# Performance work log

Hardware: AMD Instinct MI355X
Metric: run time of the kernel (lower is better)

## Reference

```python
import jax, jax.numpy as jnp
import numpy as np

TOPK = 100  # hardcoded in Block: kNNAttention(..., topk=100)
EPS = 1e-5  # torch LayerNorm default


def layer_norm(x, w, b):
    m = jnp.mean(x, axis=-1, keepdims=True)
    v = jnp.mean(jnp.square(x - m), axis=-1, keepdims=True)
    return (x - m) * jax.lax.rsqrt(v + EPS) * w + b


def setup_inputs() -> dict:
    key = jax.random.key(0)
    ks = jax.random.split(key, 8)
    B, N, C, H = 32, 512, 768, 12
    hid = 4 * C
    s_in = 1.0 / np.sqrt(C)
    s_hid = 1.0 / np.sqrt(hid)
    return {
        "x": jax.random.normal(ks[0], (B, N, C), jnp.float32),
        "islast": 0,
        "ln1_w": jnp.ones((C,), jnp.float32),
        "ln1_b": jnp.zeros((C,), jnp.float32),
        "qkv_w": jax.random.normal(ks[1], (3 * C, C), jnp.float32) * s_in,  # qkv_bias=False
        "proj_w": jax.random.normal(ks[2], (C, C), jnp.float32) * s_in,
        "proj_b": jnp.zeros((C,), jnp.float32),
        "ln2_w": jnp.ones((C,), jnp.float32),
        "ln2_b": jnp.zeros((C,), jnp.float32),
        "fc1_w": jax.random.normal(ks[3], (hid, C), jnp.float32) * s_in,
        "fc1_b": jnp.zeros((hid,), jnp.float32),
        "fc2_w": jax.random.normal(ks[4], (C, hid), jnp.float32) * s_hid,
        "fc2_b": jnp.zeros((C,), jnp.float32),
    }


def reference(x, islast, ln1_w, ln1_b, qkv_w, proj_w, proj_b, ln2_w, ln2_b, fc1_w, fc1_b, fc2_w, fc2_b):
    B, N, C = x.shape
    H = 12
    D = C // H
    scale = D ** -0.5

    # --- kNN attention on norm1(x) ---
    xn = layer_norm(x, ln1_w, ln1_b)
    qkv = (xn @ qkv_w.T).reshape(B, N, 3, H, D)
    q, k, v = (qkv[:, :, 0].transpose(0, 2, 1, 3),
               qkv[:, :, 1].transpose(0, 2, 1, 3),
               qkv[:, :, 2].transpose(0, 2, 1, 3))  # [B,H,N,D]
    attn = jnp.einsum("bhnd,bhmd->bhnm", q, k) * scale  # [B,H,N,N]
    if not bool(islast):
        # top-k mask per query row (equivalent to topk + scatter mask; ties measure-zero for floats)
        kth = jax.lax.top_k(attn, TOPK)[0][..., -1:]
        attn = jnp.where(attn >= kth, attn, -jnp.inf)
    attn = jax.nn.softmax(attn, axis=-1)
    out = jnp.einsum("bhnm,bhmd->bhnd", attn, v).transpose(0, 2, 1, 3).reshape(B, N, C)
    out = out @ proj_w.T + proj_b
    x = x + out  # residual (drop_path/dropout = 0, eval)

    # --- MLP on norm2(x) ---
    xn2 = layer_norm(x, ln2_w, ln2_b)
    h = jax.nn.gelu(xn2 @ fc1_w.T + fc1_b, approximate=False)
    x = x + (h @ fc2_w.T + fc2_b)
    return x, attn
```

## Files before the change

### kernel.cpp

```cpp
#include <hip/hip_runtime.h>
#include <hip/hip_bf16.h>
#include <math.h>

using bf16 = __hip_bfloat16;
typedef __attribute__((ext_vector_type(8))) short bh8;
typedef __attribute__((ext_vector_type(4))) float f4;

static const long long X_ELEMS = 12582912LL;

enum { EPI_F32 = 0, EPI_BIAS_RES = 2, EPI_BIAS_GELU = 3, EPI_QKV = 4, EPI_PV = 5 };

__device__ __forceinline__ float fin(float v) {
  return (fabsf(v) < 1e30f) ? v : 0.f;
}
__device__ __forceinline__ unsigned short f2bf(float f) {
  bf16 h = __float2bfloat16(f);
  return *reinterpret_cast<unsigned short*>(&h);
}
__device__ __forceinline__ uint4 pack8(float4 a, float4 b) {
  union { uint4 u; unsigned short h[8]; } r;
  r.h[0] = f2bf(a.x); r.h[1] = f2bf(a.y); r.h[2] = f2bf(a.z); r.h[3] = f2bf(a.w);
  r.h[4] = f2bf(b.x); r.h[5] = f2bf(b.y); r.h[6] = f2bf(b.z); r.h[7] = f2bf(b.w);
  return r.u;
}

__global__ __launch_bounds__(256) void cast_f32_bf16(const float* __restrict__ s,
                                                     bf16* __restrict__ d, int n4) {
  int i = blockIdx.x * 256 + threadIdx.x;
  if (i < n4) {
    float4 f = ((const float4*)s)[i];
    union { uint2 u; unsigned short h[4]; } r;
    r.h[0] = f2bf(f.x); r.h[1] = f2bf(f.y); r.h[2] = f2bf(f.z); r.h[3] = f2bf(f.w);
    ((uint2*)d)[i] = r.u;
  }
}

__global__ __launch_bounds__(256) void ln_kernel(const float* __restrict__ x,
    const float* __restrict__ w, const float* __restrict__ bi, bf16* __restrict__ out) {
  int row = blockIdx.x; int t = threadIdx.x;
  const float* xr = x + (size_t)row * 768;
  float v0 = xr[t], v1 = xr[t + 256], v2 = xr[t + 512];
  float s = v0 + v1 + v2;
  float s2 = v0 * v0 + v1 * v1 + v2 * v2;
  for (int off = 32; off; off >>= 1) { s += __shfl_down(s, off); s2 += __shfl_down(s2, off); }
  __shared__ float ls[4], ls2[4];
  int wid = t >> 6, lane = t & 63;
  if (lane == 0) { ls[wid] = s; ls2[wid] = s2; }
  __syncthreads();
  float S = ls[0] + ls[1] + ls[2] + ls[3];
  float S2 = ls2[0] + ls2[1] + ls2[2] + ls2[3];
  float mean = S * (1.0f / 768.0f);
  float var = S2 * (1.0f / 768.0f) - mean * mean;
  float rstd = rsqrtf(fmaxf(var, 0.f) + 1e-5f);
  bf16* orow = out + (size_t)row * 768;
  orow[t]       = __float2bfloat16((v0 - mean) * rstd * w[t]       + bi[t]);
  orow[t + 256] = __float2bfloat16((v1 - mean) * rstd * w[t + 256] + bi[t + 256]);
  orow[t + 512] = __float2bfloat16((v2 - mean) * rstd * w[t + 512] + bi[t + 512]);
}

template<int BN, int EPI, bool AF32>
__global__ __launch_bounds__(256)
void gemm_bt(const void* __restrict__ A, const bf16* __restrict__ B, void* __restrict__ Cout,
             int M, int N, int K,
             long long sA, long long sB, long long sC,
             const float* __restrict__ bias, const float* __restrict__ resid, float alpha,
             bf16* __restrict__ qo, bf16* __restrict__ ko, bf16* __restrict__ vo) {
  const int BM = 128, BK = 32;
  const int WN = BN / 2;
  const int NB = WN / 16;
  __shared__ unsigned short As[BM * BK];
  __shared__ unsigned short Bs[BN * BK];
  int t = threadIdx.x;
  int wid = t >> 6, lane = t & 63;
  int wm = wid >> 1, wn = wid & 1;
  int m0 = blockIdx.y * BM;
  int n0 = blockIdx.x * BN;
  int z = blockIdx.z;

  f4 acc[4][NB];
#pragma unroll
  for (int i = 0; i < 4; i++)
#pragma unroll
    for (int j = 0; j < NB; j++) acc[i][j] = f4{0.f, 0.f, 0.f, 0.f};

  int rowT = t >> 2;
  int colT = (t & 3) * 8;
  int q16 = lane >> 4;
  int r16 = lane & 15;

  for (int k0 = 0; k0 < K; k0 += BK) {
    uint4 a0, a1, b0, b1 = {0, 0, 0, 0};
    long long aoff = (long long)z * sA + (long long)(m0 + rowT) * K + (k0 + colT);
    if (AF32) {
      const float* aP = (const float*)A + aoff;
      float4 f0 = *(const float4*)aP, f1 = *(const float4*)(aP + 4);
      a0 = pack8(f0, f1);
      const float* aQ = aP + (long long)64 * K;
      f0 = *(const float4*)aQ; f1 = *(const float4*)(aQ + 4);
      a1 = pack8(f0, f1);
    } else {
      const bf16* aP = (const bf16*)A + aoff;
      a0 = *(const uint4*)aP;
      a1 = *(const uint4*)(aP + (long long)64 * K);
    }
    const bf16* bP = B + (long long)z * sB + (long long)(n0 + rowT) * K + (k0 + colT);
    b0 = *(const uint4*)bP;
    if (BN == 128) b1 = *(const uint4*)(bP + (long long)64 * K);

    __syncthreads();
    *(uint4*)&As[rowT * BK + colT] = a0;
    *(uint4*)&As[(rowT + 64) * BK + colT] = a1;
    *(uint4*)&Bs[rowT * BK + colT] = b0;
    if (BN == 128) *(uint4*)&Bs[(rowT + 64) * BK + colT] = b1;
    __syncthreads();

    bh8 af[4], bfr[NB];
#pragma unroll
    for (int i = 0; i < 4; i++) {
      int r = wm * 64 + i * 16 + r16;
      af[i] = *(const bh8*)&As[r * BK + q16 * 8];
    }
#pragma unroll
    for (int j = 0; j < NB; j++) {
      int r = wn * WN + j * 16 + r16;
      bfr[j] = *(const bh8*)&Bs[r * BK + q16 * 8];
    }
#pragma unroll
    for (int i = 0; i < 4; i++)
#pragma unroll
      for (int j = 0; j < NB; j++)
        acc[i][j] = __builtin_amdgcn_mfma_f32_16x16x32_bf16(af[i], bfr[j], acc[i][j], 0, 0, 0);
  }

  long long cbase = (long long)z * sC;
#pragma unroll
  for (int i = 0; i < 4; i++) {
#pragma unroll
    for (int j = 0; j < NB; j++) {
#pragma unroll
      for (int r = 0; r < 4; r++) {
        int mg = m0 + wm * 64 + i * 16 + q16 * 4 + r;
        int ng = n0 + wn * WN + j * 16 + r16;
        float v = acc[i][j][r] * alpha;
        if (EPI == EPI_F32) {
          ((float*)Cout)[cbase + (long long)mg * N + ng] = fin(v);
        } else if (EPI == EPI_BIAS_RES) {
          long long idx = cbase + (long long)mg * N + ng;
          v += bias[ng] + resid[idx];
          ((float*)Cout)[idx] = fin(v);
        } else if (EPI == EPI_BIAS_GELU) {
          v = fin(v + bias[ng]);
          float g = 0.5f * v * (1.0f + erff(v * 0.70710678118654752f));
          ((bf16*)Cout)[cbase + (long long)mg * N + ng] = __float2bfloat16(g);
        } else if (EPI == EPI_QKV) {
          int b = mg >> 9, n = mg & 511;
          int which = ng / 768;
          int c = ng - which * 768;
          int h = c >> 6, d = c & 63;
          size_t zz = (size_t)(b * 12 + h);
          bf16 val = __float2bfloat16(fin(v));
          if (which == 0)      qo[zz * 32768 + n * 64 + d] = val;
          else if (which == 1) ko[zz * 32768 + n * 64 + d] = val;
          else                 vo[(zz * 64 + d) * 512 + n] = val;
        } else {
          int b = z / 12, h = z - b * 12;
          ((bf16*)Cout)[((size_t)(b * 512 + mg)) * 768 + h * 64 + ng] = __float2bfloat16(fin(v));
        }
      }
    }
  }
}

__global__ __launch_bounds__(256) void topk_softmax(float* __restrict__ S,
                                                    const int* __restrict__ islast) {
  int wid = threadIdx.x >> 6, lane = threadIdx.x & 63;
  long long row = (long long)blockIdx.x * 4 + wid;
  float* sr = S + row * 512;
  float4 va = ((const float4*)sr)[lane];
  float4 vb = ((const float4*)sr)[lane + 64];
  float v[8] = {va.x, va.y, va.z, va.w, vb.x, vb.y, vb.z, vb.w};
  unsigned key[8];
  float m = -1e30f;
#pragma unroll
  for (int e = 0; e < 8; e++) {
    if (!(v[e] >= -1e38f)) v[e] = -1e38f;
    unsigned u = __float_as_uint(v[e]);
    key[e] = (u & 0x80000000u) ? ~u : (u | 0x80000000u);
    m = fmaxf(m, v[e]);
  }
  for (int off = 32; off; off >>= 1) m = fmaxf(m, __shfl_xor(m, off));

  unsigned T = 0;
  if (*islast == 0) {
    for (int bit = 31; bit >= 0; --bit) {
      unsigned Tc = T | (1u << bit);
      int cnt = 0;
#pragma unroll
      for (int e = 0; e < 8; e++) cnt += __popcll(__ballot(key[e] >= Tc));
      if (cnt >= 100) T = Tc;
      if (cnt == 100) break;
    }
  }
  float p[8]; float Z = 0.f;
#pragma unroll
  for (int e = 0; e < 8; e++) { p[e] = (key[e] >= T) ? __expf(v[e] - m) : 0.f; Z += p[e]; }
  for (int off = 32; off; off >>= 1) Z += __shfl_xor(Z, off);
  float rz = (Z > 0.f) ? (1.0f / Z) : 0.f;
  ((float4*)sr)[lane]      = float4{p[0] * rz, p[1] * rz, p[2] * rz, p[3] * rz};
  ((float4*)sr)[lane + 64] = float4{p[4] * rz, p[5] * rz, p[6] * rz, p[7] * rz};
}

extern "C" void kernel_launch(void* const* d_in, const int* in_sizes, int n_in,
                              void* d_out, int out_size, void* d_ws, size_t ws_size,
                              hipStream_t stream) {
  const float* x      = (const float*)d_in[0];
  const int*   islast = (const int*)d_in[1];
  const float* ln1_w  = (const float*)d_in[2];
  const float* ln1_b  = (const float*)d_in[3];
  const float* qkv_w  = (const float*)d_in[4];
  const float* proj_w = (const float*)d_in[5];
  const float* proj_b = (const float*)d_in[6];
  const float* ln2_w  = (const float*)d_in[7];
  const float* ln2_b  = (const float*)d_in[8];
  const float* fc1_w  = (const float*)d_in[9];
  const float* fc1_b  = (const float*)d_in[10];
  const float* fc2_w  = (const float*)d_in[11];
  const float* fc2_b  = (const float*)d_in[12];

  char* ws = (char*)d_ws;
  bf16*  wqkv = (bf16*)(ws + 0LL);
  bf16*  wproj= (bf16*)(ws + 3538944LL);
  bf16*  wfc1 = (bf16*)(ws + 4718592LL);
  bf16*  wfc2 = (bf16*)(ws + 9437184LL);
  bf16*  q    = (bf16*)(ws + 14155776LL);
  bf16*  kk   = (bf16*)(ws + 39321600LL);
  bf16*  vT   = (bf16*)(ws + 64487424LL);
  bf16*  AO   = q;
  bf16*  Hbuf = q;
  float* X1   = (float*)(ws + 39321600LL);

  float* outX    = (float*)d_out;
  float* outAttn = outX + X_ELEMS;
  bf16*  XN  = (bf16*)outX;
  bf16*  XN2 = (bf16*)((char*)d_out + 25165824LL);

  cast_f32_bf16<<<1728, 256, 0, stream>>>(qkv_w,  wqkv, 442368);
  cast_f32_bf16<<<576,  256, 0, stream>>>(proj_w, wproj, 147456);
  cast_f32_bf16<<<2304, 256, 0, stream>>>(fc1_w,  wfc1, 589824);
  cast_f32_bf16<<<2304, 256, 0, stream>>>(fc2_w,  wfc2, 589824);
  ln_kernel<<<16384, 256, 0, stream>>>(x, ln1_w, ln1_b, XN);
  gemm_bt<128, EPI_QKV, false><<<dim3(18, 128, 1), 256, 0, stream>>>(
      XN, wqkv, nullptr, 16384, 2304, 768, 0, 0, 0, nullptr, nullptr, 1.0f, q, kk, vT);
  gemm_bt<128, EPI_F32, false><<<dim3(4, 4, 384), 256, 0, stream>>>(
      q, kk, outAttn, 512, 512, 64, 32768, 32768, 262144, nullptr, nullptr, 0.125f,
      nullptr, nullptr, nullptr);
  topk_softmax<<<49152, 256, 0, stream>>>(outAttn, islast);
  gemm_bt<64, EPI_PV, true><<<dim3(1, 4, 384), 256, 0, stream>>>(
      outAttn, vT, AO, 512, 64, 512, 262144, 32768, 0, nullptr, nullptr, 1.0f,
      nullptr, nullptr, nullptr);
  gemm_bt<128, EPI_BIAS_RES, false><<<dim3(6, 128, 1), 256, 0, stream>>>(
      AO, wproj, X1, 16384, 768, 768, 0, 0, 0, proj_b, x, 1.0f, nullptr, nullptr, nullptr);
  ln_kernel<<<16384, 256, 0, stream>>>(X1, ln2_w, ln2_b, XN2);
  for (int i = 0; i < 4; ++i) {
    const bf16* xn2c = XN2 + (long long)i * 4096 * 768;
    gemm_bt<128, EPI_BIAS_GELU, false><<<dim3(24, 32, 1), 256, 0, stream>>>(
        xn2c, wfc1, Hbuf, 4096, 3072, 768, 0, 0, 0, fc1_b, nullptr, 1.0f,
        nullptr, nullptr, nullptr);
    gemm_bt<128, EPI_BIAS_RES, false><<<dim3(6, 32, 1), 256, 0, stream>>>(
        Hbuf, wfc2, outX + (long long)i * 4096 * 768, 4096, 768, 3072, 0, 0, 0,
        fc2_b, X1 + (long long)i * 4096 * 768, 1.0f, nullptr, nullptr, nullptr);
  }
  (void)in_sizes; (void)n_in; (void)out_size; (void)ws_size;
}
```

Before: 1.479 ms.

## Load GEMM bf16 tiles directly into LDS and merge weight cast kernels

The GEMM main loop now uses global_load_lds (direct global-to-LDS DMA) for bf16 A and B tiles instead of loading into registers and then storing to shared memory, followed by a vmcnt wait and a barrier. The four weight-cast launches are merged into one kernel that picks its source by index. The goal is to cut register staging and VGPR pressure and to save launch overhead. The direct-load path depends on the per-wave LDS address layout (wid*512) matching the existing As/Bs indexing. It still waits on all loads before each barrier, so no load/compute overlap is added.

```diff
diff --git a/kernel.cpp b/kernel.cpp
--- a/kernel.cpp
+++ b/kernel.cpp
@@ -23,16 +23,24 @@
   r.h[4] = f2bf(b.x); r.h[5] = f2bf(b.y); r.h[6] = f2bf(b.z); r.h[7] = f2bf(b.w);
   return r.u;
 }
-
-__global__ __launch_bounds__(256) void cast_f32_bf16(const float* __restrict__ s,
-                                                     bf16* __restrict__ d, int n4) {
+__device__ __forceinline__ void gl_lds16(const bf16* g, unsigned short* l) {
+  __builtin_amdgcn_global_load_lds((const __attribute__((address_space(1))) void*)g,
+                                   (__attribute__((address_space(3))) void*)l, 16, 0, 0);
+}
+
+__global__ __launch_bounds__(256) void cast_all(const float* __restrict__ qkv_w,
+    const float* __restrict__ proj_w, const float* __restrict__ fc1_w,
+    const float* __restrict__ fc2_w, bf16* __restrict__ dst) {
   int i = blockIdx.x * 256 + threadIdx.x;
-  if (i < n4) {
-    float4 f = ((const float4*)s)[i];
-    union { uint2 u; unsigned short h[4]; } r;
-    r.h[0] = f2bf(f.x); r.h[1] = f2bf(f.y); r.h[2] = f2bf(f.z); r.h[3] = f2bf(f.w);
-    ((uint2*)d)[i] = r.u;
-  }
+  const float* s; int base;
+  if (i < 442368)       { s = qkv_w;  base = 0; }
+  else if (i < 589824)  { s = proj_w; base = 442368; }
+  else if (i < 1179648) { s = fc1_w;  base = 589824; }
+  else                  { s = fc2_w;  base = 1179648; }
+  float4 f = ((const float4*)s)[i - base];
+  union { uint2 u; unsigned short h[4]; } r;
+  r.h[0] = f2bf(f.x); r.h[1] = f2bf(f.y); r.h[2] = f2bf(f.z); r.h[3] = f2bf(f.w);
+  ((uint2*)dst)[i] = r.u;
 }
 
 __global__ __launch_bounds__(256) void ln_kernel(const float* __restrict__ x,
@@ -88,30 +96,34 @@
   int q16 = lane >> 4;
   int r16 = lane & 15;
 
+  unsigned short* lA = As + (size_t)wid * 512;
+  unsigned short* lB = Bs + (size_t)wid * 512;
+
   for (int k0 = 0; k0 < K; k0 += BK) {
-    uint4 a0, a1, b0, b1 = {0, 0, 0, 0};
-    long long aoff = (long long)z * sA + (long long)(m0 + rowT) * K + (k0 + colT);
+    uint4 a0, a1;
     if (AF32) {
-      const float* aP = (const float*)A + aoff;
+      const float* aP = (const float*)A + (long long)z * sA + (long long)(m0 + rowT) * K + (k0 + colT);
       float4 f0 = *(const float4*)aP, f1 = *(const float4*)(aP + 4);
       a0 = pack8(f0, f1);
       const float* aQ = aP + (long long)64 * K;
       f0 = *(const float4*)aQ; f1 = *(const float4*)(aQ + 4);
       a1 = pack8(f0, f1);
+    }
+    __syncthreads();
+    if (AF32) {
+      *(uint4*)&As[rowT * BK + colT] = a0;
+      *(uint4*)&As[(rowT + 64) * BK + colT] = a1;
     } else {
-      const bf16* aP = (const bf16*)A + aoff;
-      a0 = *(const uint4*)aP;
-      a1 = *(const uint4*)(aP + (long long)64 * K);
-    }
-    const bf16* bP = B + (long long)z * sB + (long long)(n0 + rowT) * K + (k0 + colT);
-    b0 = *(const uint4*)bP;
-    if (BN == 128) b1 = *(const uint4*)(bP + (long long)64 * K);
-
-    __syncthreads();
-    *(uint4*)&As[rowT * BK + colT] = a0;
-    *(uint4*)&As[(rowT + 64) * BK + colT] = a1;
-    *(uint4*)&Bs[rowT * BK + colT] = b0;
-    if (BN == 128) *(uint4*)&Bs[(rowT + 64) * BK + colT] = b1;
+      const bf16* aP = (const bf16*)A + (long long)z * sA + (long long)(m0 + rowT) * K + (k0 + colT);
+      gl_lds16(aP, lA);
+      gl_lds16(aP + (long long)64 * K, lA + 2048);
+    }
+    {
+      const bf16* bP = B + (long long)z * sB + (long long)(n0 + rowT) * K + (k0 + colT);
+      gl_lds16(bP, lB);
+      if (BN == 128) gl_lds16(bP + (long long)64 * K, lB + 2048);
+    }
+    asm volatile("s_waitcnt vmcnt(0)" ::: "memory");
     __syncthreads();
 
     bh8 af[4], bfr[NB];
@@ -244,10 +256,7 @@
   bf16*  XN  = (bf16*)outX;
   bf16*  XN2 = (bf16*)((char*)d_out + 25165824LL);
 
-  cast_f32_bf16<<<1728, 256, 0, stream>>>(qkv_w,  wqkv, 442368);
-  cast_f32_bf16<<<576,  256, 0, stream>>>(proj_w, wproj, 147456);
-  cast_f32_bf16<<<2304, 256, 0, stream>>>(fc1_w,  wfc1, 589824);
-  cast_f32_bf16<<<2304, 256, 0, stream>>>(fc2_w,  wfc2, 589824);
+  cast_all<<<6912, 256, 0, stream>>>(qkv_w, proj_w, fc1_w, fc2_w, wqkv);
   ln_kernel<<<16384, 256, 0, stream>>>(x, ln1_w, ln1_b, XN);
   gemm_bt<128, EPI_QKV, false><<<dim3(18, 128, 1), 256, 0, stream>>>(
       XN, wqkv, nullptr, 16384, 2304, 768, 0, 0, 0, nullptr, nullptr, 1.0f, q, kk, vT);
```

Result: no change. 1.451 ms (-1.9%).
